# Optimization experiments

Measured on AMD Instinct MI355X. Metric: run time of the kernel, lower is better.

The kernel has to match this reference:

```python
import jax, jax.numpy as jnp
import numpy as np

GRID = 2
SPAN = 2.0
EMBED = 64
HIDDEN = 128
PRED_LEN = 12
N = 1024
T = 8
SCENE_SIZE = 64


def _social_pool(ht, pos, scene, active):
    """ht: [N,H], pos: [N,2], scene: [N] int, active: [N] bool -> [N, GRID*GRID, H].
    Vectorized equivalent of the per-scene scatter_add pooling: pairwise mask over
    same-scene, active, within-area, non-self pairs; bin neighbor hidden states."""
    n = ht.shape[0]
    half = SPAN / 2.0
    eps = 0.01
    rel = pos[None, :, :] - pos[:, None, :]  # rel[i,j] = pos_j - pos_i
    within = ((rel[..., 0] < half - eps) & (rel[..., 0] > -half + eps)
              & (rel[..., 1] < half - eps) & (rel[..., 1] > -half + eps))
    pair = (within & (~jnp.eye(n, dtype=bool))
            & (scene[:, None] == scene[None, :])
            & active[:, None] & active[None, :])
    cell = SPAN / GRID
    gidx = jnp.floor((rel + half) / cell).astype(jnp.int32)
    gid = jnp.clip(gidx[..., 0] * GRID + gidx[..., 1], 0, GRID * GRID - 1)
    onehot = jax.nn.one_hot(gid, GRID * GRID, dtype=ht.dtype) * pair[..., None].astype(ht.dtype)
    # pooled[i,g,h] = sum_j onehot[i,j,g] * ht[j,h]
    return jnp.einsum('ijg,jh->igh', onehot, ht)


def _lstm_step(x, h, c, Wih, Whh, bih, bhh):
    z = x @ Wih.T + bih + h @ Whh.T + bhh
    i, f, g, o = jnp.split(z, 4, axis=-1)
    c_new = jax.nn.sigmoid(f) * c + jax.nn.sigmoid(i) * jnp.tanh(g)
    h_new = jax.nn.sigmoid(o) * jnp.tanh(c_new)
    return h_new, c_new


def setup_inputs() -> dict:
    key = jax.random.key(0)
    ks = jax.random.split(key, 16)
    past_traj = jax.random.uniform(ks[0], (N, T, 2), dtype=jnp.float32) * 8.0
    past_traj_rel = jax.random.normal(ks[1], (N, T, 2), dtype=jnp.float32)
    past_traj_timestamp_mask = jnp.ones((N, T), dtype=jnp.int32)
    is_predictable = jnp.ones((N, 1), dtype=jnp.int32)
    same_scene_mask = (jnp.arange(N, dtype=jnp.int32) // SCENE_SIZE).reshape(N, 1)

    def lin(k, fan_out, fan_in):
        b = 1.0 / np.sqrt(fan_in)
        return jax.random.uniform(k, (fan_out, fan_in), jnp.float32, -b, b)

    pos_W = lin(ks[2], EMBED, 2)
    pos_b = jnp.zeros((EMBED,), jnp.float32)
    soc_W = lin(ks[3], EMBED, GRID * GRID * HIDDEN)
    soc_b = jnp.zeros((EMBED,), jnp.float32)
    Wih = lin(ks[4], 4 * HIDDEN, 2 * EMBED)
    Whh = lin(ks[5], 4 * HIDDEN, HIDDEN)
    bih = jnp.zeros((4 * HIDDEN,), jnp.float32)
    bhh = jnp.zeros((4 * HIDDEN,), jnp.float32)
    h0 = jax.random.normal(ks[6], (HIDDEN,), jnp.float32) * 0.1
    c0 = jax.random.normal(ks[7], (HIDDEN,), jnp.float32) * 0.1
    pred_W = lin(ks[8], 5, HIDDEN)
    pred_b = jnp.zeros((5,), jnp.float32)
    return {
        'past_traj': past_traj, 'past_traj_rel': past_traj_rel,
        'past_traj_timestamp_mask': past_traj_timestamp_mask,
        'is_predictable': is_predictable, 'same_scene_mask': same_scene_mask,
        'pos_W': pos_W, 'pos_b': pos_b, 'soc_W': soc_W, 'soc_b': soc_b,
        'Wih': Wih, 'Whh': Whh, 'bih': bih, 'bhh': bhh,
        'h0': h0, 'c0': c0, 'pred_W': pred_W, 'pred_b': pred_b,
    }


def reference(past_traj, past_traj_rel, past_traj_timestamp_mask, is_predictable,
              same_scene_mask, pos_W, pos_b, soc_W, soc_b, Wih, Whh, bih, bhh,
              h0, c0, pred_W, pred_b):
    n = past_traj.shape[0]
    scene = same_scene_mask[:, 0]
    ht = jnp.broadcast_to(h0[None, :], (n, HIDDEN))
    ct = jnp.broadcast_to(c0[None, :], (n, HIDDEN))

    def obs_step(carry, inp):
        ht, ct = carry
        point, rel, m = inp  # [N,2], [N,2], [N]
        active = m == 1
        pooled = _social_pool(ht, point, scene, active)  # [N,G^2,H]
        et = jax.nn.relu(rel @ pos_W.T + pos_b)
        at = jax.nn.relu(pooled.reshape(n, -1) @ soc_W.T + soc_b)
        x = jnp.concatenate([et, at], axis=-1)
        h_new, c_new = _lstm_step(x, ht, ct, Wih, Whh, bih, bhh)
        ht = jnp.where(active[:, None], h_new, ht)
        ct = jnp.where(active[:, None], c_new, ct)
        return (ht, ct), None

    obs_inp = (jnp.moveaxis(past_traj, 1, 0), jnp.moveaxis(past_traj_rel, 1, 0),
               jnp.moveaxis(past_traj_timestamp_mask, 1, 0))
    (ht, ct), _ = jax.lax.scan(obs_step, (ht, ct), obs_inp)

    pred_active = past_traj_timestamp_mask[:, -1] == 1
    pos0 = past_traj[:, -1, :]

    def pred_step(carry, _):
        ht, ct, pos = carry
        out = ht @ pred_W.T + pred_b  # [N,5]
        rel = out[:, :2]
        pos = pos + rel
        pooled = _social_pool(ht, pos, scene, pred_active)
        et = jax.nn.relu(rel @ pos_W.T + pos_b)
        at = jax.nn.relu(pooled.reshape(n, -1) @ soc_W.T + soc_b)
        x = jnp.concatenate([et, at], axis=-1)
        h_new, c_new = _lstm_step(x, ht, ct, Wih, Whh, bih, bhh)
        ht = jnp.where(pred_active[:, None], h_new, ht)
        ct = jnp.where(pred_active[:, None], c_new, ct)
        return (ht, ct, pos), (out, pos)

    (_, _, _), (outs, trajs) = jax.lax.scan(pred_step, (ht, ct, pos0), None, length=PRED_LEN)
    pred_out_all = jnp.where(pred_active[:, None, None], jnp.moveaxis(outs, 0, 1), 0.0)
    pred_traj_all = jnp.where(pred_active[:, None, None], jnp.moveaxis(trajs, 0, 1), 0.0)
    # is_predictable is all-ones in this setup, so the final boolean filter is identity
    return pred_out_all, pred_traj_all
```

## Files before the change

kernel.cpp:

```cpp
#include <hip/hip_runtime.h>

#define NAGENT 64
#define HID    128
#define TOBS   8
#define PREDL  12
#define NTHR   1024
#define XP     264
#define PP     264
#define S2P    264

typedef __attribute__((ext_vector_type(8))) short bf16x8;
typedef __attribute__((ext_vector_type(4))) short bf16x4;
typedef __attribute__((ext_vector_type(4))) float f32x4;

__device__ __forceinline__ unsigned short f2bf(float f) {
    unsigned int x = __float_as_uint(f);
    unsigned int r = (x + 0x7fffu + ((x >> 16) & 1u)) >> 16;
    return (unsigned short)r;
}
__device__ __forceinline__ float bf2f(unsigned short u) {
    return __uint_as_float(((unsigned int)u) << 16);
}
__device__ __forceinline__ float sigmf(float x) {
    return __builtin_amdgcn_rcpf(1.0f + __expf(-x));
}
__device__ __forceinline__ float tanhf_fast(float x) {
    x = fminf(fmaxf(x, -15.0f), 15.0f);
    float e = __expf(2.0f * x);
    return (e - 1.0f) * __builtin_amdgcn_rcpf(e + 1.0f);
}
__device__ __forceinline__ float sel4(float a0, float a1, float a2, float a3, int k) {
    float lo = (k & 1) ? a1 : a0;
    float hi = (k & 1) ? a3 : a2;
    return (k & 2) ? hi : lo;
}

__global__ void prep_weights(const float* __restrict__ Wih, const float* __restrict__ Whh,
                             const float* __restrict__ socW,
                             unsigned short* __restrict__ wd, unsigned short* __restrict__ wb) {
    int idx = blockIdx.x * blockDim.x + threadIdx.x;
    if (idx < 131072) {
        int e = idx & 7, l = (idx >> 3) & 63, t = idx >> 9;
        int kt = t & 7, nt = t >> 3;
        int k = kt * 32 + ((l >> 4) << 3) + e;
        int n = nt * 16 + (l & 15);
        int d = n >> 2, g = n & 3;
        int row = g * 128 + d;
        float v = (k < 128) ? Wih[row * 128 + k] : Whh[row * 128 + (k - 128)];
        wd[idx] = f2bf(v);
    } else if (idx < 163840) {
        int idx2 = idx - 131072;
        int e = idx2 & 7, l = (idx2 >> 3) & 63, t = idx2 >> 9;
        int kt = t & 3, nt = t >> 2;
        int k = kt * 32 + ((l >> 4) << 3) + e;
        int r = nt * 16 + (l & 15);
        int eo = r >> 2, g = r & 3;
        wb[idx2] = f2bf(socW[eo * 512 + g * 128 + k]);
    }
}

__global__ __launch_bounds__(NTHR) void social_lstm_mfma(
    const float* __restrict__ past_traj, const float* __restrict__ past_traj_rel,
    const int* __restrict__ ts_mask, const int* __restrict__ scene_in,
    const float* __restrict__ pos_W, const float* __restrict__ pos_b,
    const float* __restrict__ soc_b,
    const float* __restrict__ bih, const float* __restrict__ bhh,
    const float* __restrict__ h0, const float* __restrict__ c0,
    const float* __restrict__ pred_W, const float* __restrict__ pred_b,
    const unsigned short* __restrict__ wd, const unsigned short* __restrict__ wb,
    float* __restrict__ out)
{
    __shared__ __align__(16) unsigned short sh_X[NAGENT][XP];
    __shared__ __align__(16) unsigned short sh_P[NAGENT][PP];
    __shared__ __align__(16) unsigned short sh_S2[NAGENT][S2P];
    __shared__ float sh_px[NAGENT], sh_py[NAGENT], sh_rx[NAGENT], sh_ry[NAGENT];
    __shared__ float sh_o[5][NAGENT];
    __shared__ int   sh_act[NAGENT], sh_scene[NAGENT];

    const int tid  = threadIdx.x;
    const int lane = tid & 63;
    const int wv   = __builtin_amdgcn_readfirstlane(tid >> 6);
    const int gbase = blockIdx.x * NAGENT;
    const int c16 = lane & 15;
    const int q4  = lane >> 4;
    const int go  = c16 & 3;
    const int dq  = c16 >> 2;

    float bs[2], c_st[4][2], hnew[4][2];
    int dimv[2];
    #pragma unroll
    for (int s = 0; s < 2; ++s) {
        const int n = (2 * wv + s) * 16 + c16;
        const int d = n >> 2, g = n & 3;
        bs[s] = bih[g * 128 + d] + bhh[g * 128 + d];
        dimv[s] = (2 * wv + s) * 4 + dq;
        #pragma unroll
        for (int mj = 0; mj < 4; ++mj) c_st[mj][s] = c0[dimv[s]];
    }
    for (int p = tid; p < NAGENT * HID; p += NTHR) {
        int a = p >> 7, d = p & 127;
        sh_X[a][128 + d] = f2bf(h0[d]);
    }
    if (tid < NAGENT) sh_scene[tid] = scene_in[gbase + tid];
    __syncthreads();

    const bf16x8* wdp = (const bf16x8*)wd + (2 * wv * 8) * 64 + lane;
    const bf16x8* wbp = (const bf16x8*)wb + (wv * 4) * 64 + lane;
    const unsigned short* xaD = &sh_X[c16][q4 * 8];
    const unsigned short* xaB = &sh_X[c16][128 + q4 * 8];

    for (int step = 0; step < TOBS + PREDL; ++step) {
        if (step < TOBS) {
            if (tid < NAGENT) {
                const int ig = gbase + tid;
                sh_px[tid] = past_traj[(ig * TOBS + step) * 2 + 0];
                sh_py[tid] = past_traj[(ig * TOBS + step) * 2 + 1];
                sh_rx[tid] = past_traj_rel[(ig * TOBS + step) * 2 + 0];
                sh_ry[tid] = past_traj_rel[(ig * TOBS + step) * 2 + 1];
                sh_act[tid] = (ts_mask[ig * TOBS + step] == 1) ? 1 : 0;
            }
        } else {
            if (tid < 5 * NAGENT) {
                float acc = pred_b[wv];
                const float* pw = pred_W + wv * HID;
                #pragma unroll
                for (int u = 0; u < 16; ++u) {
                    const bf16x8 v = *(const bf16x8*)&sh_X[lane][128 + u * 8];
                    #pragma unroll
                    for (int e = 0; e < 8; ++e)
                        acc += bf2f((unsigned short)v[e]) * pw[u * 8 + e];
                }
                sh_o[wv][lane] = acc;
            }
            __syncthreads();
            if (tid < NAGENT) {
                const int i = tid;
                const float rx = sh_o[0][i], ry = sh_o[1][i];
                const float px = sh_px[i] + rx, py = sh_py[i] + ry;
                sh_px[i] = px; sh_py[i] = py;
                sh_rx[i] = rx; sh_ry[i] = ry;
                const float m = sh_act[i] ? 1.0f : 0.0f;
                const int p = step - TOBS;
                const int ig = gbase + i;
                float* po = out + (ig * PREDL + p) * 5;
                #pragma unroll
                for (int q = 0; q < 5; ++q) po[q] = m * sh_o[q][i];
                float* pt = out + 61440 + (ig * PREDL + p) * 2;
                pt[0] = m * px; pt[1] = m * py;
            }
        }
        __syncthreads();

        #pragma unroll
        for (int it = 0; it < 4; ++it) {
            const int p = (it << 10) + tid;
            const int i = p >> 6, j = p & 63;
            const float dx = sh_px[j] - sh_px[i];
            const float dy = sh_py[j] - sh_py[i];
            const bool within = (dx < 0.99f) & (dx > -0.99f) & (dy < 0.99f) & (dy > -0.99f);
            const bool pair = within && (i != j) && (sh_scene[i] == sh_scene[j])
                              && sh_act[i] && sh_act[j];
            int gid = (int)floorf(dx + 1.0f) * 2 + (int)floorf(dy + 1.0f);
            gid = min(max(gid, 0), 3);
            #pragma unroll
            for (int g = 0; g < 4; ++g)
                sh_P[i][g * 64 + j] = (pair && gid == g) ? (unsigned short)0x3f80
                                                         : (unsigned short)0;
        }
        {
            const float rx = sh_rx[lane], ry = sh_ry[lane];
            const int e0 = wv * 4;
            #pragma unroll
            for (int u = 0; u < 4; ++u) {
                const int e = e0 + u;
                sh_X[lane][e] = f2bf(fmaxf(pos_b[e] + rx * pos_W[e * 2] + ry * pos_W[e * 2 + 1], 0.f));
            }
        }
        {
            f32x4 acc2[4];
            #pragma unroll
            for (int mj = 0; mj < 4; ++mj) acc2[mj] = (f32x4){0.f, 0.f, 0.f, 0.f};
            #pragma unroll
            for (int kt = 0; kt < 4; ++kt) {
                const bf16x8 b = wbp[kt * 64];
                #pragma unroll
                for (int mj = 0; mj < 4; ++mj) {
                    const bf16x8 a = *(const bf16x8*)(xaB + mj * 16 * XP + kt * 32);
                    acc2[mj] = __builtin_amdgcn_mfma_f32_16x16x32_bf16(a, b, acc2[mj], 0, 0, 0);
                }
            }
            const int r = wv * 16 + c16;
            unsigned short* dst = &sh_S2[r >> 2][(r & 3) * 64 + q4 * 4];
            #pragma unroll
            for (int mj = 0; mj < 4; ++mj) {
                bf16x4 pk;
                #pragma unroll
                for (int i = 0; i < 4; ++i) pk[i] = (short)f2bf(acc2[mj][i]);
                *(bf16x4*)(dst + mj * 16) = pk;
            }
        }
        __syncthreads();

        {
            const int mt = wv & 3, nt = wv >> 2;
            f32x4 acc = (f32x4){0.f, 0.f, 0.f, 0.f};
            const unsigned short* pa = &sh_P[mt * 16 + c16][q4 * 8];
            const unsigned short* pb = &sh_S2[nt * 16 + c16][q4 * 8];
            #pragma unroll
            for (int kt = 0; kt < 8; ++kt) {
                const bf16x8 a = *(const bf16x8*)(pa + kt * 32);
                const bf16x8 b = *(const bf16x8*)(pb + kt * 32);
                acc = __builtin_amdgcn_mfma_f32_16x16x32_bf16(a, b, acc, 0, 0, 0);
            }
            const int e_ = nt * 16 + c16;
            const float sb = soc_b[e_];
            #pragma unroll
            for (int rr = 0; rr < 4; ++rr)
                sh_X[mt * 16 + q4 * 4 + rr][64 + e_] = f2bf(fmaxf(acc[rr] + sb, 0.f));
        }
        __syncthreads();

        {
            f32x4 acc[4][2];
            #pragma unroll
            for (int mj = 0; mj < 4; ++mj) {
                acc[mj][0] = (f32x4){0.f, 0.f, 0.f, 0.f};
                acc[mj][1] = (f32x4){0.f, 0.f, 0.f, 0.f};
            }
            #pragma unroll 2
            for (int kt = 0; kt < 8; ++kt) {
                const bf16x8 b0 = wdp[kt * 64];
                const bf16x8 b1 = wdp[kt * 64 + 512];
                #pragma unroll
                for (int mj = 0; mj < 4; ++mj) {
                    const bf16x8 a = *(const bf16x8*)(xaD + mj * 16 * XP + kt * 32);
                    acc[mj][0] = __builtin_amdgcn_mfma_f32_16x16x32_bf16(a, b0, acc[mj][0], 0, 0, 0);
                    acc[mj][1] = __builtin_amdgcn_mfma_f32_16x16x32_bf16(a, b1, acc[mj][1], 0, 0, 0);
                }
            }
            #pragma unroll
            for (int mj = 0; mj < 4; ++mj) {
                const int a = mj * 16 + q4 * 4 + go;
                const bool act = sh_act[a] != 0;
                #pragma unroll
                for (int s = 0; s < 2; ++s) {
                    const float z0 = acc[mj][s][0] + bs[s];
                    const float z1 = acc[mj][s][1] + bs[s];
                    const float z2 = acc[mj][s][2] + bs[s];
                    const float z3 = acc[mj][s][3] + bs[s];
                    const float s0 = sel4(z0, z1, z2, z3, go);
                    const float s1 = sel4(z0, z1, z2, z3, go ^ 1);
                    const float s2 = sel4(z0, z1, z2, z3, go ^ 2);
                    const float s3 = sel4(z0, z1, z2, z3, go ^ 3);
                    const float t1 = __shfl_xor(s1, 1, 64);
                    const float t2 = __shfl_xor(s2, 2, 64);
                    const float t3 = __shfl_xor(s3, 3, 64);
                    const float zi = sel4(s0, t1, t2, t3, go);
                    const float zf = sel4(s0, t1, t2, t3, go ^ 1);
                    const float zg = sel4(s0, t1, t2, t3, go ^ 2);
                    const float zo = sel4(s0, t1, t2, t3, go ^ 3);
                    const float cold = c_st[mj][s];
                    const float cn = sigmf(zf) * cold + sigmf(zi) * tanhf_fast(zg);
                    const float hn = sigmf(zo) * tanhf_fast(cn);
                    c_st[mj][s] = act ? cn : cold;
                    const float hold = bf2f(sh_X[a][128 + dimv[s]]);
                    hnew[mj][s] = act ? hn : hold;
                }
            }
        }
        __syncthreads();
        #pragma unroll
        for (int mj = 0; mj < 4; ++mj) {
            const int a = mj * 16 + q4 * 4 + go;
            sh_X[a][128 + dimv[0]] = f2bf(hnew[mj][0]);
            sh_X[a][128 + dimv[1]] = f2bf(hnew[mj][1]);
        }
        __syncthreads();
    }
}

extern "C" void kernel_launch(void* const* d_in, const int* in_sizes, int n_in,
                              void* d_out, int out_size, void* d_ws, size_t ws_size,
                              hipStream_t stream) {
    (void)in_sizes; (void)n_in; (void)out_size; (void)ws_size;
    unsigned short* wd = (unsigned short*)d_ws;
    unsigned short* wb = wd + 131072;
    prep_weights<<<640, 256, 0, stream>>>(
        (const float*)d_in[9], (const float*)d_in[10], (const float*)d_in[7], wd, wb);
    social_lstm_mfma<<<16, NTHR, 0, stream>>>(
        (const float*)d_in[0],
        (const float*)d_in[1],
        (const int*)  d_in[2],
        (const int*)  d_in[4],
        (const float*)d_in[5],
        (const float*)d_in[6],
        (const float*)d_in[8],
        (const float*)d_in[11],
        (const float*)d_in[12],
        (const float*)d_in[13],
        (const float*)d_in[14],
        (const float*)d_in[15],
        (const float*)d_in[16],
        wd, wb,
        (float*)d_out);
}
```

Measured before the change: 294.1 us.

## Keep LSTM weights in registers, halve threads, MFMA pred head, restructure pooling layout

```diff
diff --git a/kernel.cpp b/kernel.cpp
--- a/kernel.cpp
+++ b/kernel.cpp
@@ -4,14 +4,15 @@
 #define HID    128
 #define TOBS   8
 #define PREDL  12
-#define NTHR   1024
+#define NTHR   512
 #define XP     264
 #define PP     264
 #define S2P    264
 
 typedef __attribute__((ext_vector_type(8))) short bf16x8;
-typedef __attribute__((ext_vector_type(4))) short bf16x4;
 typedef __attribute__((ext_vector_type(4))) float f32x4;
+typedef __attribute__((ext_vector_type(4))) int   i32x4;
+typedef __attribute__((ext_vector_type(2))) unsigned int u32x2;
 
 __device__ __forceinline__ unsigned short f2bf(float f) {
     unsigned int x = __float_as_uint(f);
@@ -29,45 +30,48 @@
     float e = __expf(2.0f * x);
     return (e - 1.0f) * __builtin_amdgcn_rcpf(e + 1.0f);
 }
-__device__ __forceinline__ float sel4(float a0, float a1, float a2, float a3, int k) {
-    float lo = (k & 1) ? a1 : a0;
-    float hi = (k & 1) ? a3 : a2;
-    return (k & 2) ? hi : lo;
-}
 
 __global__ void prep_weights(const float* __restrict__ Wih, const float* __restrict__ Whh,
-                             const float* __restrict__ socW,
-                             unsigned short* __restrict__ wd, unsigned short* __restrict__ wb) {
-    int idx = blockIdx.x * blockDim.x + threadIdx.x;
+                             const float* __restrict__ socW, const float* __restrict__ predW,
+                             unsigned short* __restrict__ wd, unsigned short* __restrict__ wb,
+                             unsigned short* __restrict__ wp) {
+    int idx = blockIdx.x * 256 + threadIdx.x;
     if (idx < 131072) {
         int e = idx & 7, l = (idx >> 3) & 63, t = idx >> 9;
         int kt = t & 7, nt = t >> 3;
         int k = kt * 32 + ((l >> 4) << 3) + e;
         int n = nt * 16 + (l & 15);
-        int d = n >> 2, g = n & 3;
-        int row = g * 128 + d;
-        float v = (k < 128) ? Wih[row * 128 + k] : Whh[row * 128 + (k - 128)];
+        float v = (k < 128) ? Wih[n * 128 + k] : Whh[n * 128 + (k - 128)];
         wd[idx] = f2bf(v);
     } else if (idx < 163840) {
-        int idx2 = idx - 131072;
-        int e = idx2 & 7, l = (idx2 >> 3) & 63, t = idx2 >> 9;
+        int i2 = idx - 131072;
+        int e = i2 & 7, l = (i2 >> 3) & 63, t = i2 >> 9;
         int kt = t & 3, nt = t >> 2;
         int k = kt * 32 + ((l >> 4) << 3) + e;
         int r = nt * 16 + (l & 15);
-        int eo = r >> 2, g = r & 3;
-        wb[idx2] = f2bf(socW[eo * 512 + g * 128 + k]);
-    }
-}
-
-__global__ __launch_bounds__(NTHR) void social_lstm_mfma(
+        wb[i2] = f2bf(socW[(r >> 2) * 512 + (r & 3) * 128 + k]);
+    } else if (idx < 167936) {
+        int i3 = idx - 163840;
+        int e = i3 & 7, l = (i3 >> 3) & 63, f = i3 >> 9;
+        int kt = f & 3, half = f >> 2;
+        int k = kt * 32 + ((l >> 4) << 3) + e;
+        int n = l & 15;
+        float v = (n < 5) ? predW[n * 128 + k] : 0.0f;
+        unsigned short hi = f2bf(v);
+        wp[i3] = half ? f2bf(v - bf2f(hi)) : hi;
+    }
+}
+
+__global__ __launch_bounds__(NTHR, 2) void social_lstm_mfma(
     const float* __restrict__ past_traj, const float* __restrict__ past_traj_rel,
     const int* __restrict__ ts_mask, const int* __restrict__ scene_in,
     const float* __restrict__ pos_W, const float* __restrict__ pos_b,
     const float* __restrict__ soc_b,
     const float* __restrict__ bih, const float* __restrict__ bhh,
     const float* __restrict__ h0, const float* __restrict__ c0,
-    const float* __restrict__ pred_W, const float* __restrict__ pred_b,
+    const float* __restrict__ pred_b,
     const unsigned short* __restrict__ wd, const unsigned short* __restrict__ wb,
+    const unsigned short* __restrict__ wp,
     float* __restrict__ out)
 {
     __shared__ __align__(16) unsigned short sh_X[NAGENT][XP];
@@ -75,7 +79,8 @@
     __shared__ __align__(16) unsigned short sh_S2[NAGENT][S2P];
     __shared__ float sh_px[NAGENT], sh_py[NAGENT], sh_rx[NAGENT], sh_ry[NAGENT];
     __shared__ float sh_o[5][NAGENT];
-    __shared__ int   sh_act[NAGENT], sh_scene[NAGENT];
+    __shared__ __align__(16) int sh_act[NAGENT];
+    __shared__ int sh_scene[NAGENT];
 
     const int tid  = threadIdx.x;
     const int lane = tid & 63;
@@ -83,54 +88,59 @@
     const int gbase = blockIdx.x * NAGENT;
     const int c16 = lane & 15;
     const int q4  = lane >> 4;
-    const int go  = c16 & 3;
-    const int dq  = c16 >> 2;
-
-    float bs[2], c_st[4][2], hnew[4][2];
-    int dimv[2];
-    #pragma unroll
-    for (int s = 0; s < 2; ++s) {
-        const int n = (2 * wv + s) * 16 + c16;
-        const int d = n >> 2, g = n & 3;
-        bs[s] = bih[g * 128 + d] + bhh[g * 128 + d];
-        dimv[s] = (2 * wv + s) * 4 + dq;
-        #pragma unroll
-        for (int mj = 0; mj < 4; ++mj) c_st[mj][s] = c0[dimv[s]];
+    const int dim = wv * 16 + c16;
+
+    bf16x8 wdf[4][8];
+    {
+        const bf16x8* wdv = (const bf16x8*)wd;
+        #pragma unroll
+        for (int g = 0; g < 4; ++g)
+            #pragma unroll
+            for (int kt = 0; kt < 8; ++kt)
+                wdf[g][kt] = wdv[(((g * 8 + wv) * 8) + kt) * 64 + lane];
+    }
+    const float bs0 = bih[0 * 128 + dim] + bhh[0 * 128 + dim];
+    const float bs1 = bih[1 * 128 + dim] + bhh[1 * 128 + dim];
+    const float bs2 = bih[2 * 128 + dim] + bhh[2 * 128 + dim];
+    const float bs3 = bih[3 * 128 + dim] + bhh[3 * 128 + dim];
+    float c_reg[16];
+    {
+        const float cz = c0[dim];
+        #pragma unroll
+        for (int u = 0; u < 16; ++u) c_reg[u] = cz;
     }
     for (int p = tid; p < NAGENT * HID; p += NTHR) {
         int a = p >> 7, d = p & 127;
         sh_X[a][128 + d] = f2bf(h0[d]);
     }
-    if (tid < NAGENT) sh_scene[tid] = scene_in[gbase + tid];
+    if (tid < NAGENT) {
+        sh_scene[tid] = scene_in[gbase + tid];
+        const int ig = gbase + tid;
+        sh_px[tid] = past_traj[(ig * TOBS + 0) * 2 + 0];
+        sh_py[tid] = past_traj[(ig * TOBS + 0) * 2 + 1];
+        sh_rx[tid] = past_traj_rel[(ig * TOBS + 0) * 2 + 0];
+        sh_ry[tid] = past_traj_rel[(ig * TOBS + 0) * 2 + 1];
+        sh_act[tid] = (ts_mask[ig * TOBS + 0] == 1) ? 1 : 0;
+    }
     __syncthreads();
 
-    const bf16x8* wdp = (const bf16x8*)wd + (2 * wv * 8) * 64 + lane;
-    const bf16x8* wbp = (const bf16x8*)wb + (wv * 4) * 64 + lane;
-    const unsigned short* xaD = &sh_X[c16][q4 * 8];
-    const unsigned short* xaB = &sh_X[c16][128 + q4 * 8];
-
     for (int step = 0; step < TOBS + PREDL; ++step) {
-        if (step < TOBS) {
-            if (tid < NAGENT) {
-                const int ig = gbase + tid;
-                sh_px[tid] = past_traj[(ig * TOBS + step) * 2 + 0];
-                sh_py[tid] = past_traj[(ig * TOBS + step) * 2 + 1];
-                sh_rx[tid] = past_traj_rel[(ig * TOBS + step) * 2 + 0];
-                sh_ry[tid] = past_traj_rel[(ig * TOBS + step) * 2 + 1];
-                sh_act[tid] = (ts_mask[ig * TOBS + step] == 1) ? 1 : 0;
-            }
-        } else {
-            if (tid < 5 * NAGENT) {
-                float acc = pred_b[wv];
-                const float* pw = pred_W + wv * HID;
-                #pragma unroll
-                for (int u = 0; u < 16; ++u) {
-                    const bf16x8 v = *(const bf16x8*)&sh_X[lane][128 + u * 8];
+        if (step >= TOBS) {
+            if (wv < 4) {
+                const bf16x8* wpv = (const bf16x8*)wp;
+                f32x4 pa = (f32x4){0.f, 0.f, 0.f, 0.f};
+                #pragma unroll
+                for (int kt = 0; kt < 4; ++kt) {
+                    const bf16x8 a = *(const bf16x8*)&sh_X[wv * 16 + c16][128 + kt * 32 + q4 * 8];
+                    pa = __builtin_amdgcn_mfma_f32_16x16x32_bf16(a, wpv[kt * 64 + lane], pa, 0, 0, 0);
+                    pa = __builtin_amdgcn_mfma_f32_16x16x32_bf16(a, wpv[(4 + kt) * 64 + lane], pa, 0, 0, 0);
+                }
+                if (c16 < 5) {
+                    const float pb = pred_b[c16];
                     #pragma unroll
-                    for (int e = 0; e < 8; ++e)
-                        acc += bf2f((unsigned short)v[e]) * pw[u * 8 + e];
+                    for (int rr = 0; rr < 4; ++rr)
+                        sh_o[c16][wv * 16 + q4 * 4 + rr] = pa[rr] + pb;
                 }
-                sh_o[wv][lane] = acc;
             }
             __syncthreads();
             if (tid < NAGENT) {
@@ -148,132 +158,145 @@
                 float* pt = out + 61440 + (ig * PREDL + p) * 2;
                 pt[0] = m * px; pt[1] = m * py;
             }
-        }
-        __syncthreads();
-
-        #pragma unroll
-        for (int it = 0; it < 4; ++it) {
-            const int p = (it << 10) + tid;
+            __syncthreads();
+        }
+
+        #pragma unroll
+        for (int it = 0; it < 8; ++it) {
+            const int p = it * NTHR + tid;
             const int i = p >> 6, j = p & 63;
             const float dx = sh_px[j] - sh_px[i];
             const float dy = sh_py[j] - sh_py[i];
             const bool within = (dx < 0.99f) & (dx > -0.99f) & (dy < 0.99f) & (dy > -0.99f);
             const bool pair = within && (i != j) && (sh_scene[i] == sh_scene[j])
                               && sh_act[i] && sh_act[j];
-            int gid = (int)floorf(dx + 1.0f) * 2 + (int)floorf(dy + 1.0f);
-            gid = min(max(gid, 0), 3);
-            #pragma unroll
-            for (int g = 0; g < 4; ++g)
-                sh_P[i][g * 64 + j] = (pair && gid == g) ? (unsigned short)0x3f80
-                                                         : (unsigned short)0;
+            const int gid = ((dx >= 0.f) ? 2 : 0) + ((dy >= 0.f) ? 1 : 0);
+            unsigned int w0 = 0, w1 = 0;
+            if (pair) {
+                if (gid == 0) w0 = 0x3f80u;
+                else if (gid == 1) w0 = 0x3f800000u;
+                else if (gid == 2) w1 = 0x3f80u;
+                else w1 = 0x3f800000u;
+            }
+            u32x2 w; w[0] = w0; w[1] = w1;
+            *(u32x2*)&sh_P[i][j * 4] = w;
         }
         {
             const float rx = sh_rx[lane], ry = sh_ry[lane];
-            const int e0 = wv * 4;
-            #pragma unroll
-            for (int u = 0; u < 4; ++u) {
-                const int e = e0 + u;
-                sh_X[lane][e] = f2bf(fmaxf(pos_b[e] + rx * pos_W[e * 2] + ry * pos_W[e * 2 + 1], 0.f));
-            }
+            bf16x8 ev;
+            #pragma unroll
+            for (int u = 0; u < 8; ++u) {
+                const int e = wv * 8 + u;
+                ev[u] = (short)f2bf(fmaxf(pos_b[e] + rx * pos_W[2 * e] + ry * pos_W[2 * e + 1], 0.f));
+            }
+            *(bf16x8*)&sh_X[lane][wv * 8] = ev;
         }
         {
-            f32x4 acc2[4];
-            #pragma unroll
-            for (int mj = 0; mj < 4; ++mj) acc2[mj] = (f32x4){0.f, 0.f, 0.f, 0.f};
-            #pragma unroll
-            for (int kt = 0; kt < 4; ++kt) {
-                const bf16x8 b = wbp[kt * 64];
-                #pragma unroll
-                for (int mj = 0; mj < 4; ++mj) {
-                    const bf16x8 a = *(const bf16x8*)(xaB + mj * 16 * XP + kt * 32);
-                    acc2[mj] = __builtin_amdgcn_mfma_f32_16x16x32_bf16(a, b, acc2[mj], 0, 0, 0);
+            const bf16x8* wbv = (const bf16x8*)wb;
+            bf16x8 wbf[2][4];
+            #pragma unroll
+            for (int s = 0; s < 2; ++s)
+                #pragma unroll
+                for (int kt = 0; kt < 4; ++kt)
+                    wbf[s][kt] = wbv[((2 * wv + s) * 4 + kt) * 64 + lane];
+            #pragma unroll
+            for (int mj = 0; mj < 4; ++mj) {
+                bf16x8 a[4];
+                #pragma unroll
+                for (int kt = 0; kt < 4; ++kt)
+                    a[kt] = *(const bf16x8*)&sh_X[mj * 16 + c16][128 + kt * 32 + q4 * 8];
+                f32x4 ac[2];
+                ac[0] = (f32x4){0.f, 0.f, 0.f, 0.f};
+                ac[1] = (f32x4){0.f, 0.f, 0.f, 0.f};
+                #pragma unroll
+                for (int kt = 0; kt < 4; ++kt) {
+                    ac[0] = __builtin_amdgcn_mfma_f32_16x16x32_bf16(a[kt], wbf[0][kt], ac[0], 0, 0, 0);
+                    ac[1] = __builtin_amdgcn_mfma_f32_16x16x32_bf16(a[kt], wbf[1][kt], ac[1], 0, 0, 0);
                 }
-            }
-            const int r = wv * 16 + c16;
-            unsigned short* dst = &sh_S2[r >> 2][(r & 3) * 64 + q4 * 4];
-            #pragma unroll
-            for (int mj = 0; mj < 4; ++mj) {
-                bf16x4 pk;
-                #pragma unroll
-                for (int i = 0; i < 4; ++i) pk[i] = (short)f2bf(acc2[mj][i]);
-                *(bf16x4*)(dst + mj * 16) = pk;
+                #pragma unroll
+                for (int s = 0; s < 2; ++s) {
+                    const int r = (2 * wv + s) * 16 + c16;
+                    const int e = r >> 2, g = r & 3;
+                    #pragma unroll
+                    for (int rr = 0; rr < 4; ++rr)
+                        sh_S2[e][(mj * 16 + q4 * 4 + rr) * 4 + g] = f2bf(ac[s][rr]);
+                }
             }
         }
         __syncthreads();
 
         {
-            const int mt = wv & 3, nt = wv >> 2;
-            f32x4 acc = (f32x4){0.f, 0.f, 0.f, 0.f};
-            const unsigned short* pa = &sh_P[mt * 16 + c16][q4 * 8];
-            const unsigned short* pb = &sh_S2[nt * 16 + c16][q4 * 8];
+            const int mt = wv & 3, np = wv >> 2;
+            f32x4 ac[2];
+            ac[0] = (f32x4){0.f, 0.f, 0.f, 0.f};
+            ac[1] = (f32x4){0.f, 0.f, 0.f, 0.f};
             #pragma unroll
             for (int kt = 0; kt < 8; ++kt) {
-                const bf16x8 a = *(const bf16x8*)(pa + kt * 32);
-                const bf16x8 b = *(const bf16x8*)(pb + kt * 32);
-                acc = __builtin_amdgcn_mfma_f32_16x16x32_bf16(a, b, acc, 0, 0, 0);
-            }
-            const int e_ = nt * 16 + c16;
-            const float sb = soc_b[e_];
-            #pragma unroll
-            for (int rr = 0; rr < 4; ++rr)
-                sh_X[mt * 16 + q4 * 4 + rr][64 + e_] = f2bf(fmaxf(acc[rr] + sb, 0.f));
+                const bf16x8 a = *(const bf16x8*)&sh_P[mt * 16 + c16][kt * 32 + q4 * 8];
+                ac[0] = __builtin_amdgcn_mfma_f32_16x16x32_bf16(
+                    a, *(const bf16x8*)&sh_S2[(2 * np) * 16 + c16][kt * 32 + q4 * 8], ac[0], 0, 0, 0);
+                ac[1] = __builtin_amdgcn_mfma_f32_16x16x32_bf16(
+                    a, *(const bf16x8*)&sh_S2[(2 * np + 1) * 16 + c16][kt * 32 + q4 * 8], ac[1], 0, 0, 0);
+            }
+            #pragma unroll
+            for (int s = 0; s < 2; ++s) {
+                const int e = (2 * np + s) * 16 + c16;
+                const float sb = soc_b[e];
+                #pragma unroll
+                for (int rr = 0; rr < 4; ++rr)
+                    sh_X[mt * 16 + q4 * 4 + rr][64 + e] = f2bf(fmaxf(ac[s][rr] + sb, 0.f));
+            }
         }
         __syncthreads();
 
-        {
-            f32x4 acc[4][2];
-            #pragma unroll
-            for (int mj = 0; mj < 4; ++mj) {
-                acc[mj][0] = (f32x4){0.f, 0.f, 0.f, 0.f};
-                acc[mj][1] = (f32x4){0.f, 0.f, 0.f, 0.f};
-            }
-            #pragma unroll 2
-            for (int kt = 0; kt < 8; ++kt) {
-                const bf16x8 b0 = wdp[kt * 64];
-                const bf16x8 b1 = wdp[kt * 64 + 512];
-                #pragma unroll
-                for (int mj = 0; mj < 4; ++mj) {
-                    const bf16x8 a = *(const bf16x8*)(xaD + mj * 16 * XP + kt * 32);
-                    acc[mj][0] = __builtin_amdgcn_mfma_f32_16x16x32_bf16(a, b0, acc[mj][0], 0, 0, 0);
-                    acc[mj][1] = __builtin_amdgcn_mfma_f32_16x16x32_bf16(a, b1, acc[mj][1], 0, 0, 0);
-                }
-            }
-            #pragma unroll
-            for (int mj = 0; mj < 4; ++mj) {
-                const int a = mj * 16 + q4 * 4 + go;
-                const bool act = sh_act[a] != 0;
-                #pragma unroll
-                for (int s = 0; s < 2; ++s) {
-                    const float z0 = acc[mj][s][0] + bs[s];
-                    const float z1 = acc[mj][s][1] + bs[s];
-                    const float z2 = acc[mj][s][2] + bs[s];
-                    const float z3 = acc[mj][s][3] + bs[s];
-                    const float s0 = sel4(z0, z1, z2, z3, go);
-                    const float s1 = sel4(z0, z1, z2, z3, go ^ 1);
-                    const float s2 = sel4(z0, z1, z2, z3, go ^ 2);
-                    const float s3 = sel4(z0, z1, z2, z3, go ^ 3);
-                    const float t1 = __shfl_xor(s1, 1, 64);
-                    const float t2 = __shfl_xor(s2, 2, 64);
-                    const float t3 = __shfl_xor(s3, 3, 64);
-                    const float zi = sel4(s0, t1, t2, t3, go);
-                    const float zf = sel4(s0, t1, t2, t3, go ^ 1);
-                    const float zg = sel4(s0, t1, t2, t3, go ^ 2);
-                    const float zo = sel4(s0, t1, t2, t3, go ^ 3);
-                    const float cold = c_st[mj][s];
-                    const float cn = sigmf(zf) * cold + sigmf(zi) * tanhf_fast(zg);
-                    const float hn = sigmf(zo) * tanhf_fast(cn);
-                    c_st[mj][s] = act ? cn : cold;
-                    const float hold = bf2f(sh_X[a][128 + dimv[s]]);
-                    hnew[mj][s] = act ? hn : hold;
-                }
+        float hn_st[16];
+        unsigned int hm = 0;
+        #pragma unroll
+        for (int mj = 0; mj < 4; ++mj) {
+            bf16x8 a[8];
+            #pragma unroll
+            for (int kt = 0; kt < 8; ++kt)
+                a[kt] = *(const bf16x8*)&sh_X[mj * 16 + c16][kt * 32 + q4 * 8];
+            f32x4 acc[4];
+            #pragma unroll
+            for (int g = 0; g < 4; ++g) acc[g] = (f32x4){0.f, 0.f, 0.f, 0.f};
+            #pragma unroll
+            for (int kt = 0; kt < 8; ++kt)
+                #pragma unroll
+                for (int g = 0; g < 4; ++g)
+                    acc[g] = __builtin_amdgcn_mfma_f32_16x16x32_bf16(a[kt], wdf[g][kt], acc[g], 0, 0, 0);
+            const i32x4 a4 = *(const i32x4*)&sh_act[mj * 16 + q4 * 4];
+            #pragma unroll
+            for (int rr = 0; rr < 4; ++rr) {
+                const float zi = acc[0][rr] + bs0;
+                const float zf = acc[1][rr] + bs1;
+                const float zg = acc[2][rr] + bs2;
+                const float zo = acc[3][rr] + bs3;
+                const float cold = c_reg[mj * 4 + rr];
+                const float cn = sigmf(zf) * cold + sigmf(zi) * tanhf_fast(zg);
+                const float hn = sigmf(zo) * tanhf_fast(cn);
+                const bool act = a4[rr] != 0;
+                c_reg[mj * 4 + rr] = act ? cn : cold;
+                hn_st[mj * 4 + rr] = hn;
+                hm |= (act ? 1u : 0u) << (mj * 4 + rr);
             }
         }
         __syncthreads();
-        #pragma unroll
-        for (int mj = 0; mj < 4; ++mj) {
-            const int a = mj * 16 + q4 * 4 + go;
-            sh_X[a][128 + dimv[0]] = f2bf(hnew[mj][0]);
-            sh_X[a][128 + dimv[1]] = f2bf(hnew[mj][1]);
+
+        #pragma unroll
+        for (int u = 0; u < 16; ++u) {
+            if (hm & (1u << u)) {
+                const int mj = u >> 2, rr = u & 3;
+                sh_X[mj * 16 + q4 * 4 + rr][128 + dim] = f2bf(hn_st[u]);
+            }
+        }
+        if (step + 1 < TOBS && tid < NAGENT) {
+            const int ig = gbase + tid;
+            sh_px[tid] = past_traj[(ig * TOBS + step + 1) * 2 + 0];
+            sh_py[tid] = past_traj[(ig * TOBS + step + 1) * 2 + 1];
+            sh_rx[tid] = past_traj_rel[(ig * TOBS + step + 1) * 2 + 0];
+            sh_ry[tid] = past_traj_rel[(ig * TOBS + step + 1) * 2 + 1];
+            sh_act[tid] = (ts_mask[ig * TOBS + step + 1] == 1) ? 1 : 0;
         }
         __syncthreads();
     }
@@ -285,8 +308,10 @@
     (void)in_sizes; (void)n_in; (void)out_size; (void)ws_size;
     unsigned short* wd = (unsigned short*)d_ws;
     unsigned short* wb = wd + 131072;
-    prep_weights<<<640, 256, 0, stream>>>(
-        (const float*)d_in[9], (const float*)d_in[10], (const float*)d_in[7], wd, wb);
+    unsigned short* wp = wb + 32768;
+    prep_weights<<<656, 256, 0, stream>>>(
+        (const float*)d_in[9], (const float*)d_in[10],
+        (const float*)d_in[7], (const float*)d_in[15], wd, wb, wp);
     social_lstm_mfma<<<16, NTHR, 0, stream>>>(
         (const float*)d_in[0],
         (const float*)d_in[1],
@@ -299,8 +324,7 @@
         (const float*)d_in[12],
         (const float*)d_in[13],
         (const float*)d_in[14],
-        (const float*)d_in[15],
         (const float*)d_in[16],
-        wd, wb,
+        wd, wb, wp,
         (float*)d_out);
 }
```

New measurement: 358.6 us. 22.0% more time.
